# Optimization experiments

Hardware: AMD Instinct MI355X
Metric: run time of the kernel (lower is better)

The kernel has to match this reference:

```python
import jax, jax.numpy as jnp
import numpy as np

N_USER = 100_000
N_ITEM = 100_000
E = 1_600_000
D_IN = 64
D_OUT = 64


def setup_inputs() -> dict:
    key = jax.random.key(0)
    ks = jax.random.split(key, 14)
    inp = {
        "feat_user": jax.random.normal(ks[0], (N_USER, D_IN), jnp.float32),
        "feat_item": jax.random.normal(ks[1], (N_ITEM, D_IN), jnp.float32),
        "W_follows": jax.random.normal(ks[2], (D_OUT, D_IN), jnp.float32) * 0.05,
        "b_follows": jax.random.normal(ks[3], (D_OUT,), jnp.float32) * 0.05,
        "W_rates": jax.random.normal(ks[4], (D_OUT, D_IN), jnp.float32) * 0.05,
        "b_rates": jax.random.normal(ks[5], (D_OUT,), jnp.float32) * 0.05,
        "W_ratedby": jax.random.normal(ks[6], (D_OUT, D_IN), jnp.float32) * 0.05,
        "b_ratedby": jax.random.normal(ks[7], (D_OUT,), jnp.float32) * 0.05,
        "src_follows": jax.random.randint(ks[8], (E,), 0, N_USER, jnp.int32),
        "dst_follows": jax.random.randint(ks[9], (E,), 0, N_USER, jnp.int32),
        "src_rates": jax.random.randint(ks[10], (E,), 0, N_USER, jnp.int32),
        "dst_rates": jax.random.randint(ks[11], (E,), 0, N_ITEM, jnp.int32),
        "src_ratedby": jax.random.randint(ks[12], (E,), 0, N_ITEM, jnp.int32),
        "dst_ratedby": jax.random.randint(ks[13], (E,), 0, N_USER, jnp.int32),
    }
    return inp


def _mean_agg(Wh, src, dst, num_dst):
    # copy_u + mean: gather projected src features per edge, segment-mean into dst nodes.
    msg_sum = jax.ops.segment_sum(Wh[src], dst, num_segments=num_dst)  # [num_dst, D_OUT]
    cnt = jax.ops.segment_sum(jnp.ones(src.shape, Wh.dtype), dst, num_segments=num_dst)
    return msg_sum / jnp.maximum(cnt, 1.0)[:, None]  # zero-in-degree nodes -> 0 (DGL behavior)


def reference(feat_user, feat_item, W_follows, b_follows, W_rates, b_rates,
              W_ratedby, b_ratedby, src_follows, dst_follows, src_rates,
              dst_rates, src_ratedby, dst_ratedby):
    # Per-etype linear projection on source node features (nn.Linear: x @ W.T + b)
    Wh_f = feat_user @ W_follows.T + b_follows    # user -follows-> user
    Wh_r = feat_user @ W_rates.T + b_rates        # user -rates-> item
    Wh_rb = feat_item @ W_ratedby.T + b_ratedby   # item -rated_by-> user
    # Per-etype mean aggregation, then 'sum' cross-reducer per destination ntype
    h_user = (_mean_agg(Wh_f, src_follows, dst_follows, N_USER)
              + _mean_agg(Wh_rb, src_ratedby, dst_ratedby, N_USER))
    h_item = _mean_agg(Wh_r, src_rates, dst_rates, N_ITEM)
    return jnp.stack([h_user, h_item])  # [2, 100000, 64]
```

## Files before the change

### kernel.cpp

```cpp
#include <hip/hip_runtime.h>

#define D 64
#define NPB_SHIFT 9
#define NPB (1 << NPB_SHIFT)
#define NB 196
#define CHUNK 8192
#define HB 256

typedef float f32x4 __attribute__((ext_vector_type(4)));
typedef short bf16x8 __attribute__((ext_vector_type(8)));

__device__ __forceinline__ unsigned bf16rne(float x) {
    unsigned u = __float_as_uint(x);
    return (u + 0x7fffu + ((u >> 16) & 1u)) >> 16;
}

__global__ __launch_bounds__(256) void prep(
    const float* __restrict__ fu, const float* __restrict__ fi,
    unsigned* __restrict__ bu, unsigned* __restrict__ bi, int n4,
    const float* __restrict__ w0, const float* __restrict__ w1,
    const float* __restrict__ w2, unsigned* __restrict__ wdst,
    const int* __restrict__ d0, const int* __restrict__ d1, const int* __restrict__ d2,
    int* __restrict__ hist, int nE)
{
    const int y = blockIdx.y;
    const int bx = blockIdx.x;
    const int tid = threadIdx.x;
    if (y < 2) {
        const float4* src = y == 0 ? (const float4*)fu : (const float4*)fi;
        uint2* dst = y == 0 ? (uint2*)bu : (uint2*)bi;
        for (int i = bx * 256 + tid; i < n4; i += 2048 * 256) {
            const float4 v = src[i];
            uint2 r;
            r.x = bf16rne(v.x) | (bf16rne(v.y) << 16);
            r.y = bf16rne(v.z) | (bf16rne(v.w) << 16);
            dst[i] = r;
        }
        return;
    }
    if (bx == 0) {
        for (int i = tid; i < 3 * 2048; i += 256) {
            const int et = i >> 11, idx = i & 2047;
            const float* w = et == 0 ? w0 : (et == 1 ? w1 : w2);
            wdst[i] = bf16rne(w[2 * idx]) | (bf16rne(w[2 * idx + 1]) << 16);
        }
        return;
    }
    if (bx <= 3 * HB) {
        const int et = (bx - 1) / HB;
        const int b2 = (bx - 1) % HB;
        const int* dst = et == 0 ? d0 : (et == 1 ? d1 : d2);
        __shared__ int h[NB];
        for (int i = tid; i < NB; i += 256) h[i] = 0;
        __syncthreads();
        for (int e = b2 * 256 + tid; e < nE; e += HB * 256)
            atomicAdd(&h[dst[e] >> NPB_SHIFT], 1);
        __syncthreads();
        int* gh = hist + et * NB;
        for (int i = tid; i < NB; i += 256)
            if (h[i]) atomicAdd(&gh[i], h[i]);
    }
}

__global__ __launch_bounds__(256) void bkt_scan(
    const int* __restrict__ hist, int* __restrict__ off, int* __restrict__ gcur)
{
    const int et = blockIdx.x;
    const int tid = threadIdx.x;
    const int v = tid < NB ? hist[et * NB + tid] : 0;
    int inc = v;
#pragma unroll
    for (int of = 1; of < 64; of <<= 1) {
        int t = __shfl_up(inc, of);
        if ((tid & 63) >= of) inc += t;
    }
    __shared__ int ws[4];
    if ((tid & 63) == 63) ws[tid >> 6] = inc;
    __syncthreads();
    int woff = 0;
    for (int i = 0; i < (tid >> 6); ++i) woff += ws[i];
    const int excl = woff + inc - v;
    if (tid < NB) { off[et * NB + tid] = excl; gcur[et * NB + tid] = excl; }
}

__global__ __launch_bounds__(256) void bkt_multisplit(
    const int* __restrict__ s0, const int* __restrict__ d0,
    const int* __restrict__ s1, const int* __restrict__ d1,
    const int* __restrict__ s2, const int* __restrict__ d2,
    int* __restrict__ gcur, int* __restrict__ bkt, int nE, int E)
{
    const int et = blockIdx.y;
    const int* src = et == 0 ? s0 : (et == 1 ? s1 : s2);
    const int* dst = et == 0 ? d0 : (et == 1 ? d1 : d2);
    int* gc = gcur + et * NB;
    int* bk = bkt + (size_t)et * E;

    __shared__ int h[NB];
    __shared__ int st[NB];
    __shared__ int cu[NB];
    __shared__ int gb[NB];
    __shared__ int ws[4];
    __shared__ int stage[CHUNK];

    const int tid = threadIdx.x;
    const int e0 = blockIdx.x * CHUNK;
    const int e1 = min(e0 + CHUNK, nE);

    for (int i = tid; i < NB; i += 256) h[i] = 0;
    __syncthreads();
    for (int e = e0 + tid; e < e1; e += 256)
        atomicAdd(&h[dst[e] >> NPB_SHIFT], 1);
    __syncthreads();

    const int v = tid < NB ? h[tid] : 0;
    int inc = v;
#pragma unroll
    for (int of = 1; of < 64; of <<= 1) {
        int t = __shfl_up(inc, of);
        if ((tid & 63) >= of) inc += t;
    }
    if ((tid & 63) == 63) ws[tid >> 6] = inc;
    __syncthreads();
    int woff = 0;
    for (int i = 0; i < (tid >> 6); ++i) woff += ws[i];
    const int excl = woff + inc - v;
    if (tid < NB) {
        st[tid] = excl;
        cu[tid] = excl;
        if (v > 0) gb[tid] = atomicAdd(&gc[tid], v);
    }
    __syncthreads();

    for (int e = e0 + tid; e < e1; e += 256) {
        const int dd = dst[e];
        const int b = dd >> NPB_SHIFT;
        const int pos = atomicAdd(&cu[b], 1);
        stage[pos] = src[e] | ((dd & (NPB - 1)) << 17);
    }
    __syncthreads();

    const int wv = tid >> 6, ln = tid & 63;
    for (int b = wv; b < NB; b += 4) {
        const int cb = h[b];
        if (cb == 0) continue;
        const int base = st[b], g = gb[b];
        for (int i = ln; i < cb; i += 64)
            bk[g + i] = stage[base + i];
    }
}

__global__ __launch_bounds__(256) void bkt_csr(
    const int* __restrict__ off, const int* __restrict__ bkt_all,
    int* __restrict__ rp_all, int* __restrict__ cnt_all, int* __restrict__ lst_all,
    int N, int E)
{
    const int et = blockIdx.y;
    const int b = blockIdx.x;
    const int* o = off + et * NB;
    const int* bk = bkt_all + (size_t)et * E;
    int* lst = lst_all + (size_t)et * E;
    int* rp  = rp_all  + (size_t)et * N;
    int* cnt = cnt_all + (size_t)et * N;
    const int A  = o[b];
    const int Bb = (b + 1 < NB) ? o[b + 1] : E;

    __shared__ int h[NPB];
    __shared__ int cu[NPB];
    __shared__ int ws2[4];
    for (int i = threadIdx.x; i < NPB; i += 256) h[i] = 0;
    __syncthreads();
    for (int i = A + threadIdx.x; i < Bb; i += 256)
        atomicAdd(&h[((unsigned)bk[i]) >> 17], 1);
    __syncthreads();

    const int tid = threadIdx.x;
    const int v0 = h[2 * tid], v1 = h[2 * tid + 1];
    const int tsum = v0 + v1;
    int inc = tsum;
#pragma unroll
    for (int of = 1; of < 64; of <<= 1) {
        int t = __shfl_up(inc, of);
        if ((tid & 63) >= of) inc += t;
    }
    if ((tid & 63) == 63) ws2[tid >> 6] = inc;
    __syncthreads();
    int woff = 0;
    for (int i = 0; i < (tid >> 6); ++i) woff += ws2[i];
    const int excl = woff + inc - tsum;
    cu[2 * tid] = excl;
    cu[2 * tid + 1] = excl + v0;
    const int n0 = b << NPB_SHIFT;
    if (n0 + 2 * tid < N)     { cnt[n0 + 2 * tid]     = v0; rp[n0 + 2 * tid]     = A + excl; }
    if (n0 + 2 * tid + 1 < N) { cnt[n0 + 2 * tid + 1] = v1; rp[n0 + 2 * tid + 1] = A + excl + v0; }
    __syncthreads();

    for (int i = A + threadIdx.x; i < Bb; i += 256) {
        const int w = bk[i];
        const int dl = ((unsigned)w) >> 17;
        const int pos = atomicAdd(&cu[dl], 1);
        lst[A + pos] = w & 0x1FFFF;
    }
}

__device__ __forceinline__ void gather_mean(
    const unsigned* __restrict__ feat, const int* __restrict__ lst,
    int start, int deg, int k, int p, float& mx, float& my)
{
    float sx = 0.0f, sy = 0.0f;
    if (deg > 0) {
        int id[8];
        float mk[8];
#pragma unroll
        for (int j = 0; j < 8; ++j) {
            const int ee = 2 * j + p;
            id[j] = lst[start + (ee < deg ? ee : deg - 1)];
            mk[j] = ee < deg ? 1.0f : 0.0f;
        }
        for (int e = 0; e < deg; e += 16) {
            unsigned w[8];
#pragma unroll
            for (int j = 0; j < 8; ++j)
                w[j] = feat[id[j] * 32 + k];
            const bool more = (e + 16) < deg;
            int id2[8];
            float mk2[8];
            if (more) {
#pragma unroll
                for (int j = 0; j < 8; ++j) {
                    const int ee = e + 16 + 2 * j + p;
                    id2[j] = lst[start + (ee < deg ? ee : deg - 1)];
                    mk2[j] = ee < deg ? 1.0f : 0.0f;
                }
            }
#pragma unroll
            for (int j = 0; j < 8; ++j) {
                sx = fmaf(mk[j], __uint_as_float(w[j] << 16), sx);
                sy = fmaf(mk[j], __uint_as_float(w[j] & 0xffff0000u), sy);
            }
            if (more) {
#pragma unroll
                for (int j = 0; j < 8; ++j) { id[j] = id2[j]; mk[j] = mk2[j]; }
            }
        }
    }
    sx += __shfl_xor(sx, 32);
    sy += __shfl_xor(sy, 32);
    const float inv = deg > 0 ? 1.0f / (float)deg : 0.0f;
    mx = sx * inv;
    my = sy * inv;
}

__global__ __launch_bounds__(256) void gather_user2(
    const unsigned* __restrict__ fbu, const unsigned* __restrict__ fbi,
    const int* __restrict__ rpF, const int* __restrict__ cntF, const int* __restrict__ lstF,
    const int* __restrict__ rpR, const int* __restrict__ cntR, const int* __restrict__ lstR,
    const uint4* __restrict__ WbF, const uint4* __restrict__ WbR,
    const float* __restrict__ bF, const float* __restrict__ bR,
    float* __restrict__ out, int N)
{
    __shared__ unsigned meanL[2][16][36];
    __shared__ int degL[2][16];

    const int tid = threadIdx.x;
    const int wv = tid >> 6;
    const int l  = tid & 63;
    const int k  = l & 31;
    const int p  = l >> 5;
    const int bbase = blockIdx.x * 16;

#pragma unroll 1
    for (int et = 0; et < 2; ++et) {
        const unsigned* feat = et ? fbi : fbu;
        const int* rp  = et ? rpR  : rpF;
        const int* cnt = et ? cntR : cntF;
        const int* lst = et ? lstR : lstF;
#pragma unroll 1
        for (int q = 0; q < 4; ++q) {
            const int nl = wv * 4 + q;
            const int n = bbase + nl;
            const int deg = (n < N) ? cnt[n] : 0;
            const int start = deg > 0 ? rp[n] : 0;
            float mx, my;
            gather_mean(feat, lst, start, deg, k, p, mx, my);
            if (p == 0)
                meanL[et][nl][k] = bf16rne(mx) | (bf16rne(my) << 16);
            if (l == 0) degL[et][nl] = deg;
        }
    }
    __syncthreads();

    const int m16 = l & 15;
    const int qq  = l >> 4;
    union { uint4 u; bf16x8 v; } bf0, bf1, br0, br1, a;
    bf0.u = WbF[(wv * 16 + m16) * 8 + qq];
    bf1.u = WbF[(wv * 16 + m16) * 8 + qq + 4];
    br0.u = WbR[(wv * 16 + m16) * 8 + qq];
    br1.u = WbR[(wv * 16 + m16) * 8 + qq + 4];

    f32x4 d = {0.0f, 0.0f, 0.0f, 0.0f};
    a.u = *reinterpret_cast<const uint4*>(&meanL[0][m16][qq * 4]);
    d = __builtin_amdgcn_mfma_f32_16x16x32_bf16(a.v, bf0.v, d, 0, 0, 0);
    a.u = *reinterpret_cast<const uint4*>(&meanL[0][m16][16 + qq * 4]);
    d = __builtin_amdgcn_mfma_f32_16x16x32_bf16(a.v, bf1.v, d, 0, 0, 0);
    a.u = *reinterpret_cast<const uint4*>(&meanL[1][m16][qq * 4]);
    d = __builtin_amdgcn_mfma_f32_16x16x32_bf16(a.v, br0.v, d, 0, 0, 0);
    a.u = *reinterpret_cast<const uint4*>(&meanL[1][m16][16 + qq * 4]);
    d = __builtin_amdgcn_mfma_f32_16x16x32_bf16(a.v, br1.v, d, 0, 0, 0);

    const int o = wv * 16 + m16;
    const float boF = bF[o];
    const float boR = bR[o];
#pragma unroll
    for (int r = 0; r < 4; ++r) {
        const int nl = qq * 4 + r;
        const int gn = bbase + nl;
        if (gn < N) {
            float res = d[r];
            if (degL[0][nl] > 0) res += boF;
            if (degL[1][nl] > 0) res += boR;
            out[(size_t)gn * D + o] = res;
        }
    }
}

__global__ __launch_bounds__(256) void gather_proj_mfma(
    const unsigned* __restrict__ feat,
    const int* __restrict__ rp, const int* __restrict__ cnt, const int* __restrict__ lst,
    const uint4* __restrict__ Wb, const float* __restrict__ bias,
    float* __restrict__ out, int N)
{
    __shared__ unsigned meanL[16][36];
    __shared__ int degL[16];

    const int tid = threadIdx.x;
    const int wv = tid >> 6;
    const int l  = tid & 63;
    const int k  = l & 31;
    const int p  = l >> 5;
    const int bbase = blockIdx.x * 16;

#pragma unroll 1
    for (int q = 0; q < 4; ++q) {
        const int nl = wv * 4 + q;
        const int n = bbase + nl;
        const int deg = (n < N) ? cnt[n] : 0;
        const int start = deg > 0 ? rp[n] : 0;
        float mx, my;
        gather_mean(feat, lst, start, deg, k, p, mx, my);
        if (p == 0)
            meanL[nl][k] = bf16rne(mx) | (bf16rne(my) << 16);
        if (l == 0) degL[nl] = deg;
    }
    __syncthreads();

    const int m16 = l & 15;
    const int qq  = l >> 4;
    union { uint4 u; bf16x8 v; } b0, b1, a0, a1;
    b0.u = Wb[(wv * 16 + m16) * 8 + qq];
    b1.u = Wb[(wv * 16 + m16) * 8 + qq + 4];
    a0.u = *reinterpret_cast<const uint4*>(&meanL[m16][qq * 4]);
    a1.u = *reinterpret_cast<const uint4*>(&meanL[m16][16 + qq * 4]);

    f32x4 d = {0.0f, 0.0f, 0.0f, 0.0f};
    d = __builtin_amdgcn_mfma_f32_16x16x32_bf16(a0.v, b0.v, d, 0, 0, 0);
    d = __builtin_amdgcn_mfma_f32_16x16x32_bf16(a1.v, b1.v, d, 0, 0, 0);

    const int o = wv * 16 + m16;
    const float bo = bias[o];
#pragma unroll
    for (int r = 0; r < 4; ++r) {
        const int nl = qq * 4 + r;
        const int gn = bbase + nl;
        if (gn < N) {
            float res = d[r] + (degL[nl] > 0 ? bo : 0.0f);
            out[(size_t)gn * D + o] = res;
        }
    }
}

extern "C" void kernel_launch(void* const* d_in, const int* in_sizes, int n_in,
                              void* d_out, int out_size, void* d_ws, size_t ws_size,
                              hipStream_t stream)
{
    const float* feat_user = (const float*)d_in[0];
    const float* feat_item = (const float*)d_in[1];
    const float* W_f  = (const float*)d_in[2];
    const float* b_f  = (const float*)d_in[3];
    const float* W_r  = (const float*)d_in[4];
    const float* b_r  = (const float*)d_in[5];
    const float* W_rb = (const float*)d_in[6];
    const float* b_rb = (const float*)d_in[7];
    const int* src_f  = (const int*)d_in[8];
    const int* dst_f  = (const int*)d_in[9];
    const int* src_r  = (const int*)d_in[10];
    const int* dst_r  = (const int*)d_in[11];
    const int* src_rb = (const int*)d_in[12];
    const int* dst_rb = (const int*)d_in[13];
    float* out = (float*)d_out;

    const int NU = in_sizes[0] / D;
    const int NI = in_sizes[1] / D;
    const int E  = in_sizes[8];
    const int N  = NU;

    int* hist = (int*)d_ws;
    int* off  = hist + 3 * NB;
    int* gcur = off  + 3 * NB;
    int* rp   = gcur + 3 * NB;
    int* cnt  = rp   + 3 * (size_t)N;
    int* bkt  = cnt  + 3 * (size_t)N;
    int* lst  = bkt  + 3 * (size_t)E;
    unsigned* Wbf = (unsigned*)(lst + 3 * (size_t)E);
    unsigned* fbu = Wbf + 3 * 2048;
    unsigned* fbi = fbu + (size_t)N * 32;

    hipMemsetAsync(hist, 0, (size_t)3 * NB * sizeof(int), stream);

    const dim3 blk(256);
    const int n4 = N * D / 4;
    prep<<<dim3(2048, 3), blk, 0, stream>>>(
        feat_user, feat_item, fbu, fbi, n4,
        W_f, W_rb, W_r, Wbf,
        dst_f, dst_rb, dst_r, hist, E);
    bkt_scan<<<3, blk, 0, stream>>>(hist, off, gcur);
    const int nms = (E + CHUNK - 1) / CHUNK;
    bkt_multisplit<<<dim3(nms, 3), blk, 0, stream>>>(
        src_f, dst_f, src_rb, dst_rb, src_r, dst_r, gcur, bkt, E, E);
    bkt_csr<<<dim3(NB, 3), blk, 0, stream>>>(off, bkt, rp, cnt, lst, N, E);

    int* rp_f  = rp;            int* cnt_f  = cnt;            int* lst_f  = lst;
    int* rp_rb = rp + N;        int* cnt_rb = cnt + N;        int* lst_rb = lst + E;
    int* rp_r  = rp + 2 * N;    int* cnt_r  = cnt + 2 * N;    int* lst_r  = lst + 2 * (size_t)E;

    const int gblk = (N + 15) / 16;
    gather_user2<<<gblk, blk, 0, stream>>>(
        fbu, fbi, rp_f, cnt_f, lst_f, rp_rb, cnt_rb, lst_rb,
        (const uint4*)Wbf, (const uint4*)(Wbf + 2048), b_f, b_rb, out, NU);
    gather_proj_mfma<<<gblk, blk, 0, stream>>>(
        fbu, rp_r, cnt_r, lst_r, (const uint4*)(Wbf + 4096), b_r,
        out + (size_t)NU * D, NI);
}
```

Before: 301.8 us.

## Widen gather loads to 8-byte rows and stage bucket entries in LDS for CSR build

The per-node mean gather now has each lane load a uint2 (four bf16 features), with 16 lanes covering a row and four edges handled in parallel per wavefront. Unmasked index loads are used for full 16-edge batches, and partial sums are reduced with two cross-lane shuffles. Separately, bkt_csr copies each bucket's entries into a 36KB shared-memory buffer on the first pass, so the scatter pass reads from LDS instead of re-reading global memory. The large shared allocation may lower bkt_csr occupancy, and the wider gather adds an extra shuffle reduction step.

Result: faster. 283.7 us (-6.0%).

```diff
diff --git a/kernel.cpp b/kernel.cpp
--- a/kernel.cpp
+++ b/kernel.cpp
@@ -6,6 +6,7 @@
 #define NB 196
 #define CHUNK 8192
 #define HB 256
+#define STAGE_CAP 9216
 
 typedef float f32x4 __attribute__((ext_vector_type(4)));
 typedef short bf16x8 __attribute__((ext_vector_type(8)));
@@ -163,14 +164,26 @@
     int* cnt = cnt_all + (size_t)et * N;
     const int A  = o[b];
     const int Bb = (b + 1 < NB) ? o[b + 1] : E;
+    const int ne = Bb - A;
 
     __shared__ int h[NPB];
     __shared__ int cu[NPB];
     __shared__ int ws2[4];
+    __shared__ int stg[STAGE_CAP];
+    const bool use_stage = ne <= STAGE_CAP;
+
     for (int i = threadIdx.x; i < NPB; i += 256) h[i] = 0;
     __syncthreads();
-    for (int i = A + threadIdx.x; i < Bb; i += 256)
-        atomicAdd(&h[((unsigned)bk[i]) >> 17], 1);
+    if (use_stage) {
+        for (int i = threadIdx.x; i < ne; i += 256) {
+            const int w = bk[A + i];
+            stg[i] = w;
+            atomicAdd(&h[((unsigned)w) >> 17], 1);
+        }
+    } else {
+        for (int i = A + threadIdx.x; i < Bb; i += 256)
+            atomicAdd(&h[((unsigned)bk[i]) >> 17], 1);
+    }
     __syncthreads();
 
     const int tid = threadIdx.x;
@@ -194,64 +207,89 @@
     if (n0 + 2 * tid + 1 < N) { cnt[n0 + 2 * tid + 1] = v1; rp[n0 + 2 * tid + 1] = A + excl + v0; }
     __syncthreads();
 
-    for (int i = A + threadIdx.x; i < Bb; i += 256) {
-        const int w = bk[i];
-        const int dl = ((unsigned)w) >> 17;
-        const int pos = atomicAdd(&cu[dl], 1);
-        lst[A + pos] = w & 0x1FFFF;
-    }
-}
-
-__device__ __forceinline__ void gather_mean(
-    const unsigned* __restrict__ feat, const int* __restrict__ lst,
-    int start, int deg, int k, int p, float& mx, float& my)
-{
-    float sx = 0.0f, sy = 0.0f;
+    if (use_stage) {
+        for (int i = threadIdx.x; i < ne; i += 256) {
+            const int w = stg[i];
+            const int dl = ((unsigned)w) >> 17;
+            const int pos = atomicAdd(&cu[dl], 1);
+            lst[A + pos] = w & 0x1FFFF;
+        }
+    } else {
+        for (int i = A + threadIdx.x; i < Bb; i += 256) {
+            const int w = bk[i];
+            const int dl = ((unsigned)w) >> 17;
+            const int pos = atomicAdd(&cu[dl], 1);
+            lst[A + pos] = w & 0x1FFFF;
+        }
+    }
+}
+
+__device__ __forceinline__ void gather_mean4(
+    const uint2* __restrict__ feat, const int* __restrict__ lst,
+    int start, int deg, int k, int p, float m[4])
+{
+    float a0 = 0.0f, a1 = 0.0f, a2 = 0.0f, a3 = 0.0f;
     if (deg > 0) {
-        int id[8];
-        float mk[8];
-#pragma unroll
-        for (int j = 0; j < 8; ++j) {
-            const int ee = 2 * j + p;
-            id[j] = lst[start + (ee < deg ? ee : deg - 1)];
-            mk[j] = ee < deg ? 1.0f : 0.0f;
-        }
-        for (int e = 0; e < deg; e += 16) {
-            unsigned w[8];
-#pragma unroll
-            for (int j = 0; j < 8; ++j)
-                w[j] = feat[id[j] * 32 + k];
-            const bool more = (e + 16) < deg;
-            int id2[8];
-            float mk2[8];
+        const int nb = (deg + 15) >> 4;
+        const int rem = deg & 15;
+        int id[4];
+        float mk[4];
+        if (nb == 1 && rem) {
+#pragma unroll
+            for (int j = 0; j < 4; ++j) {
+                const int ee = 4 * j + p;
+                id[j] = lst[start + (ee < deg ? ee : deg - 1)];
+                mk[j] = ee < deg ? 1.0f : 0.0f;
+            }
+        } else {
+#pragma unroll
+            for (int j = 0; j < 4; ++j) { id[j] = lst[start + 4 * j + p]; mk[j] = 1.0f; }
+        }
+        for (int b = 0; b < nb; ++b) {
+            uint2 w[4];
+#pragma unroll
+            for (int j = 0; j < 4; ++j)
+                w[j] = feat[(size_t)id[j] * 16 + k];
+            const bool more = (b + 1) < nb;
+            int id2[4];
+            float mk2[4];
             if (more) {
-#pragma unroll
-                for (int j = 0; j < 8; ++j) {
-                    const int ee = e + 16 + 2 * j + p;
-                    id2[j] = lst[start + (ee < deg ? ee : deg - 1)];
-                    mk2[j] = ee < deg ? 1.0f : 0.0f;
+                const int e2 = (b + 1) << 4;
+                if ((b + 2 == nb) && rem) {
+#pragma unroll
+                    for (int j = 0; j < 4; ++j) {
+                        const int ee = e2 + 4 * j + p;
+                        id2[j] = lst[start + (ee < deg ? ee : deg - 1)];
+                        mk2[j] = ee < deg ? 1.0f : 0.0f;
+                    }
+                } else {
+#pragma unroll
+                    for (int j = 0; j < 4; ++j) { id2[j] = lst[start + e2 + 4 * j + p]; mk2[j] = 1.0f; }
                 }
             }
 #pragma unroll
-            for (int j = 0; j < 8; ++j) {
-                sx = fmaf(mk[j], __uint_as_float(w[j] << 16), sx);
-                sy = fmaf(mk[j], __uint_as_float(w[j] & 0xffff0000u), sy);
+            for (int j = 0; j < 4; ++j) {
+                a0 = fmaf(mk[j], __uint_as_float(w[j].x << 16), a0);
+                a1 = fmaf(mk[j], __uint_as_float(w[j].x & 0xffff0000u), a1);
+                a2 = fmaf(mk[j], __uint_as_float(w[j].y << 16), a2);
+                a3 = fmaf(mk[j], __uint_as_float(w[j].y & 0xffff0000u), a3);
             }
             if (more) {
 #pragma unroll
-                for (int j = 0; j < 8; ++j) { id[j] = id2[j]; mk[j] = mk2[j]; }
+                for (int j = 0; j < 4; ++j) { id[j] = id2[j]; mk[j] = mk2[j]; }
             }
         }
     }
-    sx += __shfl_xor(sx, 32);
-    sy += __shfl_xor(sy, 32);
+    a0 += __shfl_xor(a0, 16); a0 += __shfl_xor(a0, 32);
+    a1 += __shfl_xor(a1, 16); a1 += __shfl_xor(a1, 32);
+    a2 += __shfl_xor(a2, 16); a2 += __shfl_xor(a2, 32);
+    a3 += __shfl_xor(a3, 16); a3 += __shfl_xor(a3, 32);
     const float inv = deg > 0 ? 1.0f / (float)deg : 0.0f;
-    mx = sx * inv;
-    my = sy * inv;
+    m[0] = a0 * inv; m[1] = a1 * inv; m[2] = a2 * inv; m[3] = a3 * inv;
 }
 
 __global__ __launch_bounds__(256) void gather_user2(
-    const unsigned* __restrict__ fbu, const unsigned* __restrict__ fbi,
+    const uint2* __restrict__ fbu, const uint2* __restrict__ fbi,
     const int* __restrict__ rpF, const int* __restrict__ cntF, const int* __restrict__ lstF,
     const int* __restrict__ rpR, const int* __restrict__ cntR, const int* __restrict__ lstR,
     const uint4* __restrict__ WbF, const uint4* __restrict__ WbR,
@@ -264,13 +302,13 @@
     const int tid = threadIdx.x;
     const int wv = tid >> 6;
     const int l  = tid & 63;
-    const int k  = l & 31;
-    const int p  = l >> 5;
+    const int k  = l & 15;
+    const int p  = l >> 4;
     const int bbase = blockIdx.x * 16;
 
 #pragma unroll 1
     for (int et = 0; et < 2; ++et) {
-        const unsigned* feat = et ? fbi : fbu;
+        const uint2* feat = et ? fbi : fbu;
         const int* rp  = et ? rpR  : rpF;
         const int* cnt = et ? cntR : cntF;
         const int* lst = et ? lstR : lstF;
@@ -280,10 +318,14 @@
             const int n = bbase + nl;
             const int deg = (n < N) ? cnt[n] : 0;
             const int start = deg > 0 ? rp[n] : 0;
-            float mx, my;
-            gather_mean(feat, lst, start, deg, k, p, mx, my);
-            if (p == 0)
-                meanL[et][nl][k] = bf16rne(mx) | (bf16rne(my) << 16);
+            float m[4];
+            gather_mean4(feat, lst, start, deg, k, p, m);
+            if (p == 0) {
+                uint2 pk;
+                pk.x = bf16rne(m[0]) | (bf16rne(m[1]) << 16);
+                pk.y = bf16rne(m[2]) | (bf16rne(m[3]) << 16);
+                *reinterpret_cast<uint2*>(&meanL[et][nl][2 * k]) = pk;
+            }
             if (l == 0) degL[et][nl] = deg;
         }
     }
@@ -324,7 +366,7 @@
 }
 
 __global__ __launch_bounds__(256) void gather_proj_mfma(
-    const unsigned* __restrict__ feat,
+    const uint2* __restrict__ feat,
     const int* __restrict__ rp, const int* __restrict__ cnt, const int* __restrict__ lst,
     const uint4* __restrict__ Wb, const float* __restrict__ bias,
     float* __restrict__ out, int N)
@@ -335,8 +377,8 @@
     const int tid = threadIdx.x;
     const int wv = tid >> 6;
     const int l  = tid & 63;
-    const int k  = l & 31;
-    const int p  = l >> 5;
+    const int k  = l & 15;
+    const int p  = l >> 4;
     const int bbase = blockIdx.x * 16;
 
 #pragma unroll 1
@@ -345,10 +387,14 @@
         const int n = bbase + nl;
         const int deg = (n < N) ? cnt[n] : 0;
         const int start = deg > 0 ? rp[n] : 0;
-        float mx, my;
-        gather_mean(feat, lst, start, deg, k, p, mx, my);
-        if (p == 0)
-            meanL[nl][k] = bf16rne(mx) | (bf16rne(my) << 16);
+        float m[4];
+        gather_mean4(feat, lst, start, deg, k, p, m);
+        if (p == 0) {
+            uint2 pk;
+            pk.x = bf16rne(m[0]) | (bf16rne(m[1]) << 16);
+            pk.y = bf16rne(m[2]) | (bf16rne(m[3]) << 16);
+            *reinterpret_cast<uint2*>(&meanL[nl][2 * k]) = pk;
+        }
         if (l == 0) degL[nl] = deg;
     }
     __syncthreads();
@@ -434,9 +480,10 @@
 
     const int gblk = (N + 15) / 16;
     gather_user2<<<gblk, blk, 0, stream>>>(
-        fbu, fbi, rp_f, cnt_f, lst_f, rp_rb, cnt_rb, lst_rb,
+        (const uint2*)fbu, (const uint2*)fbi,
+        rp_f, cnt_f, lst_f, rp_rb, cnt_rb, lst_rb,
         (const uint4*)Wbf, (const uint4*)(Wbf + 2048), b_f, b_rb, out, NU);
     gather_proj_mfma<<<gblk, blk, 0, stream>>>(
-        fbu, rp_r, cnt_r, lst_r, (const uint4*)(Wbf + 4096), b_r,
+        (const uint2*)fbu, rp_r, cnt_r, lst_r, (const uint4*)(Wbf + 4096), b_r,
         out + (size_t)NU * D, NI);
 }
```
